# Kernel tuning notes

Hardware: AMD Instinct MI355X
Metric: run time of the kernel (lower is better)

The kernel has to match this reference:

```python
import jax, jax.numpy as jnp
import numpy as np

NUM_DIM = 512
NUM_ENTITIES = 200000
NUM_RELATIONS = 500
BATCH = 4096


def setup_inputs() -> dict:
    key = jax.random.key(0)
    k1, k2, k3, k4, k5, k6, k7 = jax.random.split(key, 7)
    scale = 0.02
    return {
        # Linear(1, d) per entity/relation -> weight column w and bias b; emb = w + b
        "entity_w": jax.random.normal(k1, (NUM_ENTITIES, NUM_DIM), dtype=jnp.float32) * scale,
        "entity_b": jax.random.normal(k2, (NUM_ENTITIES, NUM_DIM), dtype=jnp.float32) * scale,
        "rel_w": jax.random.normal(k3, (NUM_RELATIONS, NUM_DIM), dtype=jnp.float32) * scale,
        "rel_b": jax.random.normal(k4, (NUM_RELATIONS, NUM_DIM), dtype=jnp.float32) * scale,
        "x": jax.random.randint(k5, (BATCH,), 0, NUM_ENTITIES, dtype=jnp.int64 if jax.config.jax_enable_x64 else jnp.int32),
        "y": jax.random.randint(k6, (BATCH,), 0, NUM_ENTITIES, dtype=jnp.int64 if jax.config.jax_enable_x64 else jnp.int32),
        "r": jax.random.randint(k7, (BATCH,), 0, NUM_RELATIONS, dtype=jnp.int64 if jax.config.jax_enable_x64 else jnp.int32),
    }


def reference(entity_w, entity_b, rel_w, rel_b, x, y, r):
    d = entity_w.shape[-1]
    ent = entity_w + entity_b              # [E, d]: Linear(1,d)(ones) = w[:,0] + b
    a = ent[x]                             # [B, d] head embedding
    b = ent[y]                             # [B, d] tail embedding
    rel = rel_w[r] + rel_b[r]              # [B, d] relation embedding
    # result[i] = mean_j a[j] * b[(j-i) mod d]  (circular cross-correlation / d)
    corr = jnp.fft.irfft(jnp.conj(jnp.fft.rfft(b, axis=-1)) * jnp.fft.rfft(a, axis=-1), n=d, axis=-1) / d
    score = jnp.einsum("bd,bd->b", rel, corr)
    return jax.nn.sigmoid(score)           # [B]
```

## Files before the change

kernel.cpp:

```cpp
#include <hip/hip_runtime.h>
#include <math.h>

#define D    512
#define NW   4
#define SWZU(u) ((u) ^ ((((u) >> 4) & 3) << 2))

typedef __fp16 h8  __attribute__((ext_vector_type(8)));
typedef __fp16 h2  __attribute__((ext_vector_type(2)));
typedef float  f4_ __attribute__((ext_vector_type(4)));

__device__ __forceinline__ h2 cvt2(float lo, float hi) {
    return __builtin_amdgcn_cvt_pkrtz(lo, hi);
}
__device__ __forceinline__ unsigned pk(h2 v) { return __builtin_bit_cast(unsigned, v); }
__device__ __forceinline__ unsigned ab16(unsigned hi, unsigned lo) {
    return __builtin_amdgcn_alignbit(hi, lo, 16);
}

__global__ __launch_bounds__(256, 6) void hole_mfma_kernel(
    const float* __restrict__ ew, const float* __restrict__ eb,
    const float* __restrict__ rw, const float* __restrict__ rb,
    const int* __restrict__ xs, const int* __restrict__ ys,
    const int* __restrict__ rs, float* __restrict__ out)
{
    __shared__ uint4 smem[NW][392];

    const int w    = threadIdx.x >> 6;
    const int l    = threadIdx.x & 63;
    const int mn   = l & 15;
    const int hq   = l >> 4;
    const int item = blockIdx.x * NW + w;

    const int xi = xs[item], yi = ys[item], ri = rs[item];
    uint4* S = smem[w];

    {
        const float4* yw4 = (const float4*)(ew + (size_t)yi * D);
        const float4* yb4 = (const float4*)(eb + (size_t)yi * D);
        float4 b0 = yw4[2*l], b1 = yw4[2*l+1], b2 = yb4[2*l], b3 = yb4[2*l+1];
        uint4 vb;
        vb.x = pk(cvt2(b0.x+b2.x, b0.y+b2.y)); vb.y = pk(cvt2(b0.z+b2.z, b0.w+b2.w));
        vb.z = pk(cvt2(b1.x+b3.x, b1.y+b3.y)); vb.w = pk(cvt2(b1.z+b3.z, b1.w+b3.w));
        const int s0 = SWZU(2*l) >> 1;
        S[s0]      = vb;
        S[s0 + 64] = vb;
    }

    {
        const float4* xw4 = (const float4*)(ew + (size_t)xi * D);
        const float4* xb4 = (const float4*)(eb + (size_t)xi * D);
        float4 a0 = xw4[2*l], a1 = xw4[2*l+1], a2 = xb4[2*l], a3 = xb4[2*l+1];
        uint4 va;
        va.x = pk(cvt2(a0.x+a2.x, a0.y+a2.y)); va.y = pk(cvt2(a0.z+a2.z, a0.w+a2.w));
        va.z = pk(cvt2(a1.x+a3.x, a1.y+a3.y)); va.w = pk(cvt2(a1.z+a3.z, a1.w+a3.w));

        const unsigned nx1 = (unsigned)__shfl((int)va.x, (l + 1) & 63, 64);
        const unsigned nx2 = (unsigned)__shfl((int)va.y, (l + 1) & 63, 64);
        uint4 c1, c2, c3;
        c1.x = ab16(va.y, va.x); c1.y = ab16(va.z, va.y);
        c1.z = ab16(va.w, va.z); c1.w = ab16(nx1,  va.w);
        c2.x = va.y; c2.y = va.z; c2.z = va.w; c2.w = nx1;
        c3.x = ab16(va.z, va.y); c3.y = ab16(va.w, va.z);
        c3.z = ab16(nx1,  va.w); c3.w = ab16(nx2,  nx1);
        S[128 + l]       = va;
        S[128 + 66 + l]  = c1;
        S[128 + 132 + l] = c2;
        S[128 + 198 + l] = c3;
        if (l < 2) {
            S[128 + 64 + l]       = va;
            S[128 + 66 + 64 + l]  = c1;
            S[128 + 132 + 64 + l] = c2;
            S[128 + 198 + 64 + l] = c3;
        }
    }

    const uint2* W = (const uint2*)S;
    int lu = 128 + hq - 4 * mn;
    int ub = 256 + 132 * (mn & 3) + hq + (mn >> 2);

    f4_ acc0 = {0.f, 0.f, 0.f, 0.f};
    f4_ acc1 = {0.f, 0.f, 0.f, 0.f};

    #pragma unroll
    for (int t = 0; t < 16; ++t) {
        const int s0 = SWZU(lu), s1 = SWZU(lu + 4);
        const uint2 p00 = W[s0],      p01 = W[s1];
        const uint2 p10 = W[s0 - 64], p11 = W[s1 - 64];
        const uint2 q0  = W[ub],      q1  = W[ub + 4];

        const h8 af0 = __builtin_bit_cast(h8, make_uint4(p00.x, p00.y, p01.x, p01.y));
        const h8 af1 = __builtin_bit_cast(h8, make_uint4(p10.x, p10.y, p11.x, p11.y));
        const h8 bf  = __builtin_bit_cast(h8, make_uint4(q0.x,  q0.y,  q1.x,  q1.y));

        acc0 = __builtin_amdgcn_mfma_f32_16x16x32_f16(af0, bf, acc0, 0, 0, 0);
        acc1 = __builtin_amdgcn_mfma_f32_16x16x32_f16(af1, bf, acc1, 0, 0, 0);

        lu += 8; ub += 8;
    }

    const float* rwrow = rw + (size_t)ri * D;
    const float* rbrow = rb + (size_t)ri * D;
    const int ridx = 64 * hq + mn;
    float part = 0.f;
    #pragma unroll
    for (int q = 0; q < 4; ++q) {
        const float rv0 = rwrow[ridx + 16*q]       + rbrow[ridx + 16*q];
        const float rv1 = rwrow[ridx + 16*q + 256] + rbrow[ridx + 16*q + 256];
        part += rv0 * acc0[q] + rv1 * acc1[q];
    }

    #pragma unroll
    for (int off = 32; off >= 1; off >>= 1) part += __shfl_down(part, off, 64);

    if (l == 0)
        out[item] = 1.0f / (1.0f + expf(-part * (1.0f / (float)D)));
}

extern "C" void kernel_launch(void* const* d_in, const int* in_sizes, int n_in,
                              void* d_out, int out_size, void* d_ws, size_t ws_size,
                              hipStream_t stream)
{
    const float* ew = (const float*)d_in[0];
    const float* eb = (const float*)d_in[1];
    const float* rw = (const float*)d_in[2];
    const float* rb = (const float*)d_in[3];
    const int*   xs = (const int*)d_in[4];
    const int*   ys = (const int*)d_in[5];
    const int*   rs = (const int*)d_in[6];
    float* out = (float*)d_out;

    const int batch = in_sizes[4];
    dim3 grid(batch / NW), block(NW * 64);
    hole_mfma_kernel<<<grid, block, 0, stream>>>(ew, eb, rw, rb, xs, ys, rs, out);
}
```

Before: 13.84 us.

## Process two items per wave and prefetch second item's rows during first MFMA

Each wave now handles two batch items. The second item's entity rows are gathered before the first item's MFMA loop runs, so their global-memory latency can overlap compute. The grid is halved and launch bounds lowered to allow more registers for the prefetched data. This reduces the number of resident waves available to hide latency, and the shared staging buffer is reused without a barrier, relying on in-order LDS access within a wave.

Result: slower. 15.02 us (+8.6%).

```diff
diff --git a/kernel.cpp b/kernel.cpp
--- a/kernel.cpp
+++ b/kernel.cpp
@@ -3,6 +3,7 @@
 
 #define D    512
 #define NW   4
+#define NIT  2
 #define SWZU(u) ((u) ^ ((((u) >> 4) & 3) << 2))
 
 typedef __fp16 h8  __attribute__((ext_vector_type(8)));
@@ -17,69 +18,55 @@
     return __builtin_amdgcn_alignbit(hi, lo, 16);
 }
 
-__global__ __launch_bounds__(256, 6) void hole_mfma_kernel(
-    const float* __restrict__ ew, const float* __restrict__ eb,
-    const float* __restrict__ rw, const float* __restrict__ rb,
-    const int* __restrict__ xs, const int* __restrict__ ys,
-    const int* __restrict__ rs, float* __restrict__ out)
+__device__ __forceinline__ uint4 gather_row(const float* __restrict__ tw,
+                                            const float* __restrict__ tb,
+                                            int row, int l)
 {
-    __shared__ uint4 smem[NW][392];
+    const float4* w4 = (const float4*)(tw + (size_t)row * D);
+    const float4* b4 = (const float4*)(tb + (size_t)row * D);
+    float4 a0 = w4[2*l], a1 = w4[2*l+1], a2 = b4[2*l], a3 = b4[2*l+1];
+    uint4 v;
+    v.x = pk(cvt2(a0.x+a2.x, a0.y+a2.y)); v.y = pk(cvt2(a0.z+a2.z, a0.w+a2.w));
+    v.z = pk(cvt2(a1.x+a3.x, a1.y+a3.y)); v.w = pk(cvt2(a1.z+a3.z, a1.w+a3.w));
+    return v;
+}
 
-    const int w    = threadIdx.x >> 6;
-    const int l    = threadIdx.x & 63;
-    const int mn   = l & 15;
-    const int hq   = l >> 4;
-    const int item = blockIdx.x * NW + w;
+__device__ __forceinline__ void stage_item(uint4* __restrict__ S, int l,
+                                           uint4 vb, uint4 va)
+{
+    const int s0 = SWZU(2*l) >> 1;
+    S[s0]      = vb;
+    S[s0 + 64] = vb;
 
-    const int xi = xs[item], yi = ys[item], ri = rs[item];
-    uint4* S = smem[w];
+    const unsigned nx1 = (unsigned)__shfl((int)va.x, (l + 1) & 63, 64);
+    const unsigned nx2 = (unsigned)__shfl((int)va.y, (l + 1) & 63, 64);
+    uint4 c1, c2, c3;
+    c1.x = ab16(va.y, va.x); c1.y = ab16(va.z, va.y);
+    c1.z = ab16(va.w, va.z); c1.w = ab16(nx1,  va.w);
+    c2.x = va.y; c2.y = va.z; c2.z = va.w; c2.w = nx1;
+    c3.x = ab16(va.z, va.y); c3.y = ab16(va.w, va.z);
+    c3.z = ab16(nx1,  va.w); c3.w = ab16(nx2,  nx1);
+    S[128 + l]       = va;
+    S[128 + 66 + l]  = c1;
+    S[128 + 132 + l] = c2;
+    S[128 + 198 + l] = c3;
+    if (l < 2) {
+        S[128 + 64 + l]       = va;
+        S[128 + 66 + 64 + l]  = c1;
+        S[128 + 132 + 64 + l] = c2;
+        S[128 + 198 + 64 + l] = c3;
+    }
+}
 
-    {
-        const float4* yw4 = (const float4*)(ew + (size_t)yi * D);
-        const float4* yb4 = (const float4*)(eb + (size_t)yi * D);
-        float4 b0 = yw4[2*l], b1 = yw4[2*l+1], b2 = yb4[2*l], b3 = yb4[2*l+1];
-        uint4 vb;
-        vb.x = pk(cvt2(b0.x+b2.x, b0.y+b2.y)); vb.y = pk(cvt2(b0.z+b2.z, b0.w+b2.w));
-        vb.z = pk(cvt2(b1.x+b3.x, b1.y+b3.y)); vb.w = pk(cvt2(b1.z+b3.z, b1.w+b3.w));
-        const int s0 = SWZU(2*l) >> 1;
-        S[s0]      = vb;
-        S[s0 + 64] = vb;
-    }
-
-    {
-        const float4* xw4 = (const float4*)(ew + (size_t)xi * D);
-        const float4* xb4 = (const float4*)(eb + (size_t)xi * D);
-        float4 a0 = xw4[2*l], a1 = xw4[2*l+1], a2 = xb4[2*l], a3 = xb4[2*l+1];
-        uint4 va;
-        va.x = pk(cvt2(a0.x+a2.x, a0.y+a2.y)); va.y = pk(cvt2(a0.z+a2.z, a0.w+a2.w));
-        va.z = pk(cvt2(a1.x+a3.x, a1.y+a3.y)); va.w = pk(cvt2(a1.z+a3.z, a1.w+a3.w));
-
-        const unsigned nx1 = (unsigned)__shfl((int)va.x, (l + 1) & 63, 64);
-        const unsigned nx2 = (unsigned)__shfl((int)va.y, (l + 1) & 63, 64);
-        uint4 c1, c2, c3;
-        c1.x = ab16(va.y, va.x); c1.y = ab16(va.z, va.y);
-        c1.z = ab16(va.w, va.z); c1.w = ab16(nx1,  va.w);
-        c2.x = va.y; c2.y = va.z; c2.z = va.w; c2.w = nx1;
-        c3.x = ab16(va.z, va.y); c3.y = ab16(va.w, va.z);
-        c3.z = ab16(nx1,  va.w); c3.w = ab16(nx2,  nx1);
-        S[128 + l]       = va;
-        S[128 + 66 + l]  = c1;
-        S[128 + 132 + l] = c2;
-        S[128 + 198 + l] = c3;
-        if (l < 2) {
-            S[128 + 64 + l]       = va;
-            S[128 + 66 + 64 + l]  = c1;
-            S[128 + 132 + 64 + l] = c2;
-            S[128 + 198 + 64 + l] = c3;
-        }
-    }
-
+__device__ __forceinline__ void mfma_item(const uint4* __restrict__ S,
+                                          int mn, int hq, f4_& acc0, f4_& acc1)
+{
     const uint2* W = (const uint2*)S;
     int lu = 128 + hq - 4 * mn;
     int ub = 256 + 132 * (mn & 3) + hq + (mn >> 2);
 
-    f4_ acc0 = {0.f, 0.f, 0.f, 0.f};
-    f4_ acc1 = {0.f, 0.f, 0.f, 0.f};
+    acc0 = (f4_){0.f, 0.f, 0.f, 0.f};
+    acc1 = (f4_){0.f, 0.f, 0.f, 0.f};
 
     #pragma unroll
     for (int t = 0; t < 16; ++t) {
@@ -97,23 +84,71 @@
 
         lu += 8; ub += 8;
     }
+}
 
-    const float* rwrow = rw + (size_t)ri * D;
-    const float* rbrow = rb + (size_t)ri * D;
+__global__ __launch_bounds__(NW * 64, 4) void hole_mfma_kernel(
+    const float* __restrict__ ew, const float* __restrict__ eb,
+    const float* __restrict__ rw, const float* __restrict__ rb,
+    const int* __restrict__ xs, const int* __restrict__ ys,
+    const int* __restrict__ rs, float* __restrict__ out)
+{
+    __shared__ uint4 smem[NW][392];
+
+    const int w  = threadIdx.x >> 6;
+    const int l  = threadIdx.x & 63;
+    const int mn = l & 15;
+    const int hq = l >> 4;
+    const int i0 = (blockIdx.x * NW + w) * NIT;
+
+    const int x0 = xs[i0],   y0 = ys[i0],   r0 = rs[i0];
+    const int x1 = xs[i0+1], y1 = ys[i0+1], r1 = rs[i0+1];
+
+    uint4* S = smem[w];
     const int ridx = 64 * hq + mn;
-    float part = 0.f;
+    const float* rw0 = rw + (size_t)r0 * D, *rb0 = rb + (size_t)r0 * D;
+    const float* rw1 = rw + (size_t)r1 * D, *rb1 = rb + (size_t)r1 * D;
+
+    const uint4 vb0 = gather_row(ew, eb, y0, l);
+    const uint4 va0 = gather_row(ew, eb, x0, l);
+    stage_item(S, l, vb0, va0);
+
+    const uint4 vb1 = gather_row(ew, eb, y1, l);
+    const uint4 va1 = gather_row(ew, eb, x1, l);
+    float rv0[8];
     #pragma unroll
     for (int q = 0; q < 4; ++q) {
-        const float rv0 = rwrow[ridx + 16*q]       + rbrow[ridx + 16*q];
-        const float rv1 = rwrow[ridx + 16*q + 256] + rbrow[ridx + 16*q + 256];
-        part += rv0 * acc0[q] + rv1 * acc1[q];
+        rv0[q]   = rw0[ridx + 16*q]       + rb0[ridx + 16*q];
+        rv0[4+q] = rw0[ridx + 16*q + 256] + rb0[ridx + 16*q + 256];
     }
 
+    f4_ acc0, acc1;
+    mfma_item(S, mn, hq, acc0, acc1);
+
+    {
+        float part = acc0[0]*rv0[0] + acc0[1]*rv0[1] + acc0[2]*rv0[2] + acc0[3]*rv0[3]
+                   + acc1[0]*rv0[4] + acc1[1]*rv0[5] + acc1[2]*rv0[6] + acc1[3]*rv0[7];
+        #pragma unroll
+        for (int off = 32; off >= 1; off >>= 1) part += __shfl_down(part, off, 64);
+        if (l == 0) out[i0] = 1.0f / (1.0f + expf(-part * (1.0f / (float)D)));
+    }
+
+    stage_item(S, l, vb1, va1);
+
+    float rv1[8];
     #pragma unroll
-    for (int off = 32; off >= 1; off >>= 1) part += __shfl_down(part, off, 64);
+    for (int q = 0; q < 4; ++q) {
+        rv1[q]   = rw1[ridx + 16*q]       + rb1[ridx + 16*q];
+        rv1[4+q] = rw1[ridx + 16*q + 256] + rb1[ridx + 16*q + 256];
+    }
 
-    if (l == 0)
-        out[item] = 1.0f / (1.0f + expf(-part * (1.0f / (float)D)));
+    mfma_item(S, mn, hq, acc0, acc1);
+    {
+        float part = acc0[0]*rv1[0] + acc0[1]*rv1[1] + acc0[2]*rv1[2] + acc0[3]*rv1[3]
+                   + acc1[0]*rv1[4] + acc1[1]*rv1[5] + acc1[2]*rv1[6] + acc1[3]*rv1[7];
+        #pragma unroll
+        for (int off = 32; off >= 1; off >>= 1) part += __shfl_down(part, off, 64);
+        if (l == 0) out[i0+1] = 1.0f / (1.0f + expf(-part * (1.0f / (float)D)));
+    }
 }
 
 extern "C" void kernel_launch(void* const* d_in, const int* in_sizes, int n_in,
@@ -130,6 +165,6 @@
     float* out = (float*)d_out;
 
     const int batch = in_sizes[4];
-    dim3 grid(batch / NW), block(NW * 64);
+    dim3 grid(batch / (NW * NIT)), block(NW * 64);
     hole_mfma_kernel<<<grid, block, 0, stream>>>(ew, eb, rw, rb, xs, ys, rs, out);
 }
```
